# Performance work log

Measured on AMD Instinct MI355X. Metric: run time of the kernel, lower is better.

The kernel has to match this reference:

```python
import jax, jax.numpy as jnp
import numpy as np
import math

B, T, C = 4, 2048, 1024
H = 16
HD = C // H


def setup_inputs() -> dict:
    key = jax.random.key(0)
    k1, k2, k3 = jax.random.split(key, 3)
    sc = 0.02
    return {
        "x": jax.random.normal(k1, (B, T, C), dtype=jnp.float32),
        "w_qkv": jax.random.normal(k2, (3 * C, C), dtype=jnp.float32) * sc,
        "b_qkv": jnp.zeros((3 * C,), dtype=jnp.float32),
        "w_proj": jax.random.normal(k3, (C, C), dtype=jnp.float32) * sc,
        "b_proj": jnp.zeros((C,), dtype=jnp.float32),
    }


def reference(x, w_qkv, b_qkv, w_proj, b_proj):
    b, t, c = x.shape
    qkv = x @ w_qkv.T + b_qkv            # [B,T,3C]
    q, k, v = jnp.split(qkv, 3, axis=2)
    # [B,T,C] -> [B,H,T,HD]
    def heads(z):
        return z.reshape(b, t, H, HD).transpose(0, 2, 1, 3)
    q, k, v = heads(q), heads(k), heads(v)
    att = jnp.einsum('bhqd,bhkd->bhqk', q, k) / math.sqrt(HD)
    causal = jnp.tril(jnp.ones((t, t), dtype=bool))
    att = jnp.where(causal[None, None], att, -jnp.inf)
    att = jax.nn.softmax(att, axis=-1)   # dropout p=0 (eval)
    y = jnp.einsum('bhqk,bhkd->bhqd', att, v)
    y = y.transpose(0, 2, 1, 3).reshape(b, t, c)
    return y @ w_proj.T + b_proj
```

## Files before the change

### kernel.cpp

```cpp
#include <hip/hip_runtime.h>
#include <hip/hip_bf16.h>

#define B_ 4
#define T_ 2048
#define C_ 1024
#define H_ 16
#define HD_ 64
#define M_ (B_*T_)

typedef __attribute__((ext_vector_type(8))) short short8;
typedef __attribute__((ext_vector_type(4))) float f32x4;
typedef __attribute__((ext_vector_type(16))) float f32x16;
typedef __attribute__((ext_vector_type(4))) unsigned int u32x4;
typedef unsigned short u16;
typedef unsigned int u32;

__device__ __forceinline__ u16 f2bf(float f){
  unsigned int x = __builtin_bit_cast(unsigned int, f);
  x += 0x7fffu + ((x >> 16) & 1u);
  return (u16)(x >> 16);
}

__device__ __forceinline__ u32 cvtpk(float lo, float hi){
  u32 r;
  asm("v_cvt_pk_bf16_f32 %0, %1, %2" : "=v"(r) : "v"(lo), "v"(hi));
  return r;
}

__global__ __launch_bounds__(256) void cvt_kernel(const float* __restrict__ in,
                                                  u16* __restrict__ out, int n4){
  int i = blockIdx.x * 256 + threadIdx.x;
  if (i >= n4) return;
  float4 f = reinterpret_cast<const float4*>(in)[i];
  ushort4 u;
  u.x = f2bf(f.x); u.y = f2bf(f.y); u.z = f2bf(f.z); u.w = f2bf(f.w);
  reinterpret_cast<ushort4*>(out)[i] = u;
}

template<int MODE>
__global__ __launch_bounds__(256)
void gemm_bt(const u16* __restrict__ A, const u16* __restrict__ Bt,
             const float* __restrict__ bias, float* __restrict__ Cf,
             u16* __restrict__ Qo, u16* __restrict__ Ko, u16* __restrict__ Vo,
             int N, int K)
{
  __shared__ u16 As[128][72];
  __shared__ u16 Bs[128][72];
  const int tid = threadIdx.x;
  const int wave = tid >> 6, lane = tid & 63;
  const int lo = lane & 15, hi = lane >> 4;
  const int wm = (wave >> 1) * 64, wn = (wave & 1) * 64;
  const long bm = (long)blockIdx.y * 128, bn = (long)blockIdx.x * 128;

  f32x4 acc[4][4];
  #pragma unroll
  for (int i = 0; i < 4; i++)
    #pragma unroll
    for (int j = 0; j < 4; j++)
      acc[i][j] = (f32x4){0.f, 0.f, 0.f, 0.f};

  const int r = tid >> 3;
  const int ccol = (tid & 7) * 8;

  for (int k0 = 0; k0 < K; k0 += 64){
    if (k0) __syncthreads();
    #pragma unroll
    for (int rr = 0; rr < 4; rr++){
      int row = r + rr * 32;
      *reinterpret_cast<short8*>(&As[row][ccol]) =
        *reinterpret_cast<const short8*>(&A[(bm + row) * K + k0 + ccol]);
      *reinterpret_cast<short8*>(&Bs[row][ccol]) =
        *reinterpret_cast<const short8*>(&Bt[(bn + row) * K + k0 + ccol]);
    }
    __syncthreads();
    #pragma unroll
    for (int kk = 0; kk < 64; kk += 32){
      short8 af[4], bf[4];
      #pragma unroll
      for (int mi = 0; mi < 4; mi++)
        af[mi] = *reinterpret_cast<const short8*>(&As[wm + mi*16 + lo][kk + hi*8]);
      #pragma unroll
      for (int ni = 0; ni < 4; ni++)
        bf[ni] = *reinterpret_cast<const short8*>(&Bs[wn + ni*16 + lo][kk + hi*8]);
      #pragma unroll
      for (int mi = 0; mi < 4; mi++)
        #pragma unroll
        for (int ni = 0; ni < 4; ni++)
          acc[mi][ni] = __builtin_amdgcn_mfma_f32_16x16x32_bf16(af[mi], bf[ni], acc[mi][ni], 0, 0, 0);
    }
  }

  #pragma unroll
  for (int mi = 0; mi < 4; mi++){
    #pragma unroll
    for (int ni = 0; ni < 4; ni++){
      #pragma unroll
      for (int rg = 0; rg < 4; rg++){
        long rowg = bm + wm + mi*16 + hi*4 + rg;
        long colg = bn + wn + ni*16 + lo;
        float v = acc[mi][ni][rg] + bias[colg];
        if (MODE == 0){
          int part = (int)(colg >> 10), cc = (int)(colg & 1023);
          int h = cc >> 6, d = cc & 63;
          long b = rowg >> 11, t = rowg & 2047;
          if (part == 0) v *= 0.18033688f;
          u16* dst = (part == 0) ? Qo : ((part == 1) ? Ko : Vo);
          dst[(((b << 4) + h) * 2048 + t) * 64 + d] = f2bf(v);
        } else {
          Cf[rowg * (long)N + colg] = v;
        }
      }
    }
  }
}

__global__ __launch_bounds__(256)
void vtrans_kernel(const u16* __restrict__ V, u16* __restrict__ Vt){
  __shared__ u16 Ls[64][72];
  const int bh = blockIdx.y;
  const int t0 = blockIdx.x * 64;
  const u16* Vb = V + ((size_t)bh * 2048 + t0) * 64;
  u16* Ob = Vt + (size_t)bh * 64 * 2048 + t0;
  const int r = threadIdx.x >> 3;
  const int c = (threadIdx.x & 7) * 8;
  #pragma unroll
  for (int rr = 0; rr < 64; rr += 32){
    int row = r + rr;
    *reinterpret_cast<short8*>(&Ls[row][c ^ (((row >> 4) & 3) << 4)]) =
      *reinterpret_cast<const short8*>(&Vb[(size_t)row * 64 + c]);
  }
  __syncthreads();
  const int d  = threadIdx.x >> 2;
  const int tc = (threadIdx.x & 3) * 16;
  const int v  = ((tc >> 4) & 3) << 4;
  short8 o0, o1;
  #pragma unroll
  for (int j = 0; j < 8; j++) o0[j] = (short)Ls[tc + j][d ^ v];
  #pragma unroll
  for (int j = 0; j < 8; j++) o1[j] = (short)Ls[tc + 8 + j][d ^ v];
  *reinterpret_cast<short8*>(&Ob[(size_t)d * 2048 + tc]) = o0;
  *reinterpret_cast<short8*>(&Ob[(size_t)d * 2048 + tc + 8]) = o1;
}

__global__ __launch_bounds__(128, 4)
void attn_kernel(const u16* __restrict__ Q, const u16* __restrict__ K,
                 const u16* __restrict__ Vt, u16* __restrict__ Y)
{
  const int blk = blockIdx.x;
  const int bh = blk & 63;
  const int g  = blk >> 6;
  const int tid = threadIdx.x, wave = tid >> 6, lane = tid & 63;
  const int l31 = lane & 31, h5 = lane >> 5;
  const int qc = wave ? (63 - g) : g;
  const int q0w = qc * 32;
  const int qrow = q0w + l31;
  const u16* Qb = Q  + (size_t)bh * 2048 * 64;
  const u16* Kb = K  + (size_t)bh * 2048 * 64;
  const u16* Vb = Vt + (size_t)bh * 64 * 2048;

  short8 qf[4];
  #pragma unroll
  for (int ks = 0; ks < 4; ks++)
    qf[ks] = *reinterpret_cast<const short8*>(&Qb[(size_t)qrow * 64 + ks * 16 + h5 * 8]);

  f32x16 o0, o1;
  #pragma unroll
  for (int i = 0; i < 16; i++){ o0[i] = 0.f; o1[i] = 0.f; }
  float m = -1e30f, l = 0.f;

  const int F = qc >> 1;

  for (int jt = 0; jt <= F; jt++){
    const int k0 = jt << 6;

    short8 kf0[4], kf1[4];
    #pragma unroll
    for (int ks = 0; ks < 4; ks++){
      kf0[ks] = *reinterpret_cast<const short8*>(&Kb[(size_t)(k0 + l31) * 64 + ks * 16 + h5 * 8]);
      kf1[ks] = *reinterpret_cast<const short8*>(&Kb[(size_t)(k0 + 32 + l31) * 64 + ks * 16 + h5 * 8]);
    }
    f32x16 st0, st1;
    #pragma unroll
    for (int i = 0; i < 16; i++){ st0[i] = 0.f; st1[i] = 0.f; }
    #pragma unroll
    for (int ks = 0; ks < 4; ks++)
      st0 = __builtin_amdgcn_mfma_f32_32x32x16_bf16(kf0[ks], qf[ks], st0, 0, 0, 0);
    #pragma unroll
    for (int ks = 0; ks < 4; ks++)
      st1 = __builtin_amdgcn_mfma_f32_32x32x16_bf16(kf1[ks], qf[ks], st1, 0, 0, 0);

    short8 vf0[4], vf1[4];
    #pragma unroll
    for (int ks = 0; ks < 4; ks++){
      vf0[ks] = *reinterpret_cast<const short8*>(&Vb[(size_t)l31 * 2048 + k0 + ks * 16 + h5 * 8]);
      vf1[ks] = *reinterpret_cast<const short8*>(&Vb[(size_t)(32 + l31) * 2048 + k0 + ks * 16 + h5 * 8]);
    }

    if (jt == F){
      #pragma unroll
      for (int r = 0; r < 16; r++){
        int kvr = k0 + (r & 3) + 8 * (r >> 2) + 4 * h5;
        if (kvr > qrow)      st0[r] = -1e30f;
        if (kvr + 32 > qrow) st1[r] = -1e30f;
      }
    }

    float t[16];
    #pragma unroll
    for (int r = 0; r < 16; r++) t[r] = fmaxf(st0[r], st1[r]);
    #pragma unroll
    for (int s = 8; s > 0; s >>= 1)
      #pragma unroll
      for (int r = 0; r < 8; r++) if (r < s) t[r] = fmaxf(t[r], t[r + s]);
    float rm = fmaxf(t[0], __shfl_xor(t[0], 32));
    float mn = fmaxf(m, rm);
    float alpha = __builtin_amdgcn_exp2f(m - mn);
    m = mn;
    float rs = 0.f;
    #pragma unroll
    for (int r = 0; r < 16; r++){
      st0[r] = __builtin_amdgcn_exp2f(st0[r] - mn);
      st1[r] = __builtin_amdgcn_exp2f(st1[r] - mn);
      rs += st0[r] + st1[r];
    }
    rs += __shfl_xor(rs, 32);
    l = l * alpha + rs;
    #pragma unroll
    for (int i = 0; i < 16; i++){ o0[i] *= alpha; o1[i] *= alpha; }

    short8 pa[4];
    #pragma unroll
    for (int ks2 = 0; ks2 < 4; ks2++){
      const f32x16& sv = (ks2 < 2) ? st0 : st1;
      const int gg = 8 * (ks2 & 1);
      u32 w0 = cvtpk(sv[gg + 0], sv[gg + 1]);
      u32 w1 = cvtpk(sv[gg + 2], sv[gg + 3]);
      u32 w2 = cvtpk(sv[gg + 4], sv[gg + 5]);
      u32 w3 = cvtpk(sv[gg + 6], sv[gg + 7]);
      u32 sa = h5 ? w0 : w2;
      u32 sb = h5 ? w1 : w3;
      u32 ra = (u32)__shfl_xor((int)sa, 32);
      u32 rb = (u32)__shfl_xor((int)sb, 32);
      u32x4 pw;
      pw.x = h5 ? ra : w0;
      pw.y = h5 ? rb : w1;
      pw.z = h5 ? w2 : ra;
      pw.w = h5 ? w3 : rb;
      pa[ks2] = __builtin_bit_cast(short8, pw);
    }

    #pragma unroll
    for (int ks = 0; ks < 4; ks++)
      o0 = __builtin_amdgcn_mfma_f32_32x32x16_bf16(vf0[ks], pa[ks], o0, 0, 0, 0);
    #pragma unroll
    for (int ks = 0; ks < 4; ks++)
      o1 = __builtin_amdgcn_mfma_f32_32x32x16_bf16(vf1[ks], pa[ks], o1, 0, 0, 0);
  }

  const int b = bh >> 4, h = bh & 15;
  const float inv = 1.f / l;
  u16* Yr = Y + ((size_t)(b * 2048 + qrow)) * 1024 + h * 64;
  #pragma unroll
  for (int rq = 0; rq < 4; rq++){
    ushort4 ua, ub;
    #pragma unroll
    for (int e = 0; e < 4; e++){
      ((u16*)&ua)[e] = f2bf(o0[rq * 4 + e] * inv);
      ((u16*)&ub)[e] = f2bf(o1[rq * 4 + e] * inv);
    }
    *reinterpret_cast<ushort4*>(&Yr[rq * 8 + h5 * 4])      = ua;
    *reinterpret_cast<ushort4*>(&Yr[32 + rq * 8 + h5 * 4]) = ub;
  }
}

extern "C" void kernel_launch(void* const* d_in, const int* in_sizes, int n_in,
                              void* d_out, int out_size, void* d_ws, size_t ws_size,
                              hipStream_t stream)
{
  const float* x      = (const float*)d_in[0];
  const float* w_qkv  = (const float*)d_in[1];
  const float* b_qkv  = (const float*)d_in[2];
  const float* w_proj = (const float*)d_in[3];
  const float* b_proj = (const float*)d_in[4];
  float* out = (float*)d_out;

  char* ws = (char*)d_ws;
  u16* xb     = (u16*)(ws);
  u16* wqkvb  = (u16*)(ws + (16u << 20));
  u16* wprojb = (u16*)(ws + (22u << 20));
  u16* qb     = (u16*)(ws + (24u << 20));
  u16* kb     = (u16*)(ws + (40u << 20));
  u16* vb     = (u16*)(ws + (56u << 20));
  u16* yb     = (u16*)(ws + (72u << 20));
  u16* vtb    = xb;

  int nx  = B_ * T_ * C_ / 4;
  int nw1 = 3 * C_ * C_ / 4;
  int nw2 = C_ * C_ / 4;
  cvt_kernel<<<(nx  + 255) / 256, 256, 0, stream>>>(x,      xb,     nx);
  cvt_kernel<<<(nw1 + 255) / 256, 256, 0, stream>>>(w_qkv,  wqkvb,  nw1);
  cvt_kernel<<<(nw2 + 255) / 256, 256, 0, stream>>>(w_proj, wprojb, nw2);

  dim3 g1(3072 / 128, M_ / 128);
  gemm_bt<0><<<g1, 256, 0, stream>>>(xb, wqkvb, b_qkv, nullptr, qb, kb, vb, 3072, C_);

  dim3 gt(T_ / 64, B_ * H_);
  vtrans_kernel<<<gt, 256, 0, stream>>>(vb, vtb);

  attn_kernel<<<2048, 128, 0, stream>>>(qb, kb, vtb, yb);

  dim3 g2(1024 / 128, M_ / 128);
  gemm_bt<1><<<g2, 256, 0, stream>>>(yb, wprojb, b_proj, out, nullptr, nullptr, nullptr, C_, C_);
}
```

Before: 284.5 us.

## Load GEMM tiles via global_load_lds and regroup attention into 4-wave blocks

The GEMM now stages A and B tiles with direct global-to-LDS loads instead of going through registers, and drops the padded LDS layout in favour of a dense 64-wide row stride. The attention kernel moves from 2-wave blocks that pair complementary causal query chunks to 4-wave blocks holding consecutive query chunks, with a permuted batch-head mapping. The direct loads cut register traffic, but the unpadded LDS rows may cause bank conflicts on the MFMA fragment reads. The new attention grouping gives up the causal load balancing within a block.

```diff
diff --git a/kernel.cpp b/kernel.cpp
--- a/kernel.cpp
+++ b/kernel.cpp
@@ -26,6 +26,10 @@
   asm("v_cvt_pk_bf16_f32 %0, %1, %2" : "=v"(r) : "v"(lo), "v"(hi));
   return r;
 }
+
+#define GLOAD_LDS(gsrc, ldst) \
+  __builtin_amdgcn_global_load_lds((const __attribute__((address_space(1))) u32*)(gsrc), \
+                                   (__attribute__((address_space(3))) u32*)(ldst), 16, 0, 0)
 
 __global__ __launch_bounds__(256) void cvt_kernel(const float* __restrict__ in,
                                                   u16* __restrict__ out, int n4){
@@ -44,8 +48,8 @@
              u16* __restrict__ Qo, u16* __restrict__ Ko, u16* __restrict__ Vo,
              int N, int K)
 {
-  __shared__ u16 As[128][72];
-  __shared__ u16 Bs[128][72];
+  __shared__ u16 As[128 * 64];
+  __shared__ u16 Bs[128 * 64];
   const int tid = threadIdx.x;
   const int wave = tid >> 6, lane = tid & 63;
   const int lo = lane & 15, hi = lane >> 4;
@@ -59,18 +63,14 @@
     for (int j = 0; j < 4; j++)
       acc[i][j] = (f32x4){0.f, 0.f, 0.f, 0.f};
 
-  const int r = tid >> 3;
-  const int ccol = (tid & 7) * 8;
-
   for (int k0 = 0; k0 < K; k0 += 64){
     if (k0) __syncthreads();
     #pragma unroll
-    for (int rr = 0; rr < 4; rr++){
-      int row = r + rr * 32;
-      *reinterpret_cast<short8*>(&As[row][ccol]) =
-        *reinterpret_cast<const short8*>(&A[(bm + row) * K + k0 + ccol]);
-      *reinterpret_cast<short8*>(&Bs[row][ccol]) =
-        *reinterpret_cast<const short8*>(&Bt[(bn + row) * K + k0 + ccol]);
+    for (int j = 0; j < 4; j++){
+      int chunk = j * 256 + tid;
+      int row = chunk >> 3, cc = (chunk & 7) * 8;
+      GLOAD_LDS(&A [(bm + row) * K + k0 + cc], &As[chunk * 8]);
+      GLOAD_LDS(&Bt[(bn + row) * K + k0 + cc], &Bs[chunk * 8]);
     }
     __syncthreads();
     #pragma unroll
@@ -78,10 +78,10 @@
       short8 af[4], bf[4];
       #pragma unroll
       for (int mi = 0; mi < 4; mi++)
-        af[mi] = *reinterpret_cast<const short8*>(&As[wm + mi*16 + lo][kk + hi*8]);
+        af[mi] = *reinterpret_cast<const short8*>(&As[(wm + mi*16 + lo) * 64 + kk + hi*8]);
       #pragma unroll
       for (int ni = 0; ni < 4; ni++)
-        bf[ni] = *reinterpret_cast<const short8*>(&Bs[wn + ni*16 + lo][kk + hi*8]);
+        bf[ni] = *reinterpret_cast<const short8*>(&Bs[(wn + ni*16 + lo) * 64 + kk + hi*8]);
       #pragma unroll
       for (int mi = 0; mi < 4; mi++)
         #pragma unroll
@@ -142,16 +142,16 @@
   *reinterpret_cast<short8*>(&Ob[(size_t)d * 2048 + tc + 8]) = o1;
 }
 
-__global__ __launch_bounds__(128, 4)
+__global__ __launch_bounds__(256, 2)
 void attn_kernel(const u16* __restrict__ Q, const u16* __restrict__ K,
                  const u16* __restrict__ Vt, u16* __restrict__ Y)
 {
   const int blk = blockIdx.x;
-  const int bh = blk & 63;
-  const int g  = blk >> 6;
+  const int bh = (blk & 7) * 8 + ((blk >> 3) & 7);
+  const int qg = blk >> 6;
   const int tid = threadIdx.x, wave = tid >> 6, lane = tid & 63;
   const int l31 = lane & 31, h5 = lane >> 5;
-  const int qc = wave ? (63 - g) : g;
+  const int qc = qg * 4 + wave;
   const int q0w = qc * 32;
   const int qrow = q0w + l31;
   const u16* Qb = Q  + (size_t)bh * 2048 * 64;
@@ -307,7 +307,7 @@
   dim3 gt(T_ / 64, B_ * H_);
   vtrans_kernel<<<gt, 256, 0, stream>>>(vb, vtb);
 
-  attn_kernel<<<2048, 128, 0, stream>>>(qb, kb, vtb, yb);
+  attn_kernel<<<1024, 256, 0, stream>>>(qb, kb, vtb, yb);
 
   dim3 g2(1024 / 128, M_ / 128);
   gemm_bt<1><<<g2, 256, 0, stream>>>(yb, wprojb, b_proj, out, nullptr, nullptr, nullptr, C_, C_);
```

After: 274.3 us. -3.6%, faster.
